# Kernel optimization log

Hardware: AMD Instinct MI355X
Metric: run time of the kernel (lower is better)

Reference implementation:

```python
import jax, jax.numpy as jnp
import numpy as np

B, LH, LP = 128, 64, 8
COV, TRE, OUT = 16, 8, 4
H = 128
H2 = 2 * H  # SDE latent dim
THETA, MU_SDE, SIGMA = 1.0, 0.0, 0.5
DT = 0.05
SUB = 20  # substeps per unit time interval (dt=0.05)
NSTEPS = (LP - 1) * SUB
EPS = 1e-5


def _tstats(x):
    # stats over the time axis (dim_to_normalize=-2)
    return x.mean(axis=1, keepdims=True), x.std(axis=1, keepdims=True)


def _ln(x):
    m = x.mean(-1, keepdims=True)
    v = ((x - m) ** 2).mean(-1, keepdims=True)
    return (x - m) * jax.lax.rsqrt(v + EPS)


def _gru_dir(x, Wih, Whh, bih, bhh):
    # x: (B, L, I); torch GRU gate order r, z, n
    gi_all = jnp.einsum('blc,gc->blg', x, Wih) + bih  # (B, L, 3H)

    def step(h, gi):
        gh = h @ Whh.T + bhh
        ir, iz, inn = jnp.split(gi, 3, axis=-1)
        hr, hz, hn = jnp.split(gh, 3, axis=-1)
        r = jax.nn.sigmoid(ir + hr)
        z = jax.nn.sigmoid(iz + hz)
        n = jnp.tanh(inn + r * hn)
        return (1.0 - z) * n + z * h, None

    h0 = jnp.zeros((x.shape[0], Whh.shape[1]), x.dtype)
    hT, _ = jax.lax.scan(step, h0, jnp.swapaxes(gi_all, 0, 1))
    return hT


def _bigru_hidden(x, Wf, Uf, bf, cf, Wb, Ub, bb, cb):
    # bidirectional GRU, hidden.mean(0) over the two directions
    return 0.5 * (_gru_dir(x, Wf, Uf, bf, cf) + _gru_dir(x[:, ::-1], Wb, Ub, bb, cb))


def _drift(y, mlp):
    # MLP [2H,4H,4H,2H], Linear -> Tanh -> LayerNorm per layer
    for W, b, g, be in mlp:
        y = _ln(jnp.tanh(y @ W.T + b)) * g + be
    return y


def setup_inputs():
    key = jax.random.key(0)
    ki = iter(jax.random.split(key, 64))
    nx = lambda shape, s=1.0: jax.random.normal(next(ki), shape, jnp.float32) * s
    d = {}
    d['covariate_history'] = nx((B, LH, COV))
    d['treatment_history'] = nx((B, LH, TRE))
    d['outcome_history'] = nx((B, LH, OUT))
    d['treatments'] = nx((B, LP, TRE))
    d['outcomes'] = nx((B, LP, OUT))
    for pre, insz in (('enc', COV + TRE + OUT), ('dec', TRE)):
        for suf in ('f', 'b'):
            d[f'{pre}_Wih_{suf}'] = nx((3 * H, insz), 0.05)
            d[f'{pre}_Whh_{suf}'] = nx((3 * H, H), 0.05)
            d[f'{pre}_bih_{suf}'] = jnp.zeros((3 * H,), jnp.float32)
            d[f'{pre}_bhh_{suf}'] = jnp.zeros((3 * H,), jnp.float32)
    dims = [H2, 2 * H2, 2 * H2, H2]
    for i in range(3):
        d[f'mlp_W{i}'] = nx((dims[i + 1], dims[i]), 0.05)
        d[f'mlp_b{i}'] = jnp.zeros((dims[i + 1],), jnp.float32)
        d[f'mlp_g{i}'] = jnp.ones((dims[i + 1],), jnp.float32)
        d[f'mlp_be{i}'] = jnp.zeros((dims[i + 1],), jnp.float32)
    d['out_W'] = nx((2 * OUT, H), 0.05)
    d['out_b'] = jnp.zeros((2 * OUT,), jnp.float32)
    d['ln_var_w'] = jnp.ones((OUT,), jnp.float32)
    d['ln_var_b'] = jnp.zeros((OUT,), jnp.float32)
    d['noise'] = nx((NSTEPS, B, H2))  # Brownian increments (pre-drawn)
    return d


def reference(covariate_history, treatment_history, outcome_history, treatments, outcomes,
              enc_Wih_f, enc_Whh_f, enc_bih_f, enc_bhh_f, enc_Wih_b, enc_Whh_b, enc_bih_b, enc_bhh_b,
              dec_Wih_f, dec_Whh_f, dec_bih_f, dec_bhh_f, dec_Wih_b, dec_Whh_b, dec_bih_b, dec_bhh_b,
              mlp_W0, mlp_b0, mlp_g0, mlp_be0, mlp_W1, mlp_b1, mlp_g1, mlp_be1,
              mlp_W2, mlp_b2, mlp_g2, mlp_be2, out_W, out_b, ln_var_w, ln_var_b, noise):
    # fixed (non-learned) time-axis normalizations
    om, os_ = _tstats(outcome_history)
    oh = (outcome_history - om) / (os_ + EPS)
    tm, ts_ = _tstats(treatment_history)
    tr = (treatments - tm) / (ts_ + EPS)
    th = (treatment_history - tm) / (ts_ + EPS)
    cm, cs = _tstats(covariate_history)
    ch = (covariate_history - cm) / (cs + EPS)

    enc_in = jnp.concatenate([ch, th, oh], axis=-1)  # (B, LH, COV+TRE+OUT)
    enc_h = _bigru_hidden(enc_in, enc_Wih_f, enc_Whh_f, enc_bih_f, enc_bhh_f,
                          enc_Wih_b, enc_Whh_b, enc_bih_b, enc_bhh_b)
    dec_h = _bigru_hidden(tr, dec_Wih_f, dec_Whh_f, dec_bih_f, dec_bhh_f,
                          dec_Wih_b, dec_Whh_b, dec_bih_b, dec_bhh_b)

    x0 = jnp.concatenate([enc_h, dec_h], axis=-1)  # (B, H2)
    aug0 = jnp.concatenate([x0, jnp.zeros((x0.shape[0], 1), x0.dtype)], axis=-1)
    mlp = ((mlp_W0, mlp_b0, mlp_g0, mlp_be0), (mlp_W1, mlp_b1, mlp_g1, mlp_be1),
           (mlp_W2, mlp_b2, mlp_g2, mlp_be2))
    sq = jnp.float32(np.sqrt(DT))

    def sde_step(y, nz):
        ys_ = y[:, :H2]
        f = _drift(ys_, mlp)
        u = (f - THETA * (MU_SDE - ys_)) / SIGMA
        flq = 0.5 * jnp.sum(u * u, axis=-1, keepdims=True)
        ynew = jnp.concatenate([ys_ + f * DT + (SIGMA * sq) * nz,
                                y[:, H2:] + flq * DT], axis=-1)
        return ynew, ynew

    _, traj = jax.lax.scan(sde_step, aug0, noise)
    ys = jnp.concatenate([aug0[None], traj[SUB - 1::SUB]], axis=0)  # (LP, B, H2+1)

    y = jnp.swapaxes(ys[..., :H], 0, 1)               # (B, LP, H) - first H dims only (as in source)
    logqp = jnp.transpose(ys[..., H:], (1, 2, 0))     # (B, H+1, LP)

    dec_out = y @ out_W.T + out_b                     # (B, LP, 2*OUT)
    mu_o, var_o = jnp.split(dec_out, 2, axis=-1)
    vm = var_o.mean(axis=1, keepdims=True)
    vv = var_o.var(axis=1, keepdims=True)
    var = jax.nn.sigmoid((var_o - vm) * jax.lax.rsqrt(vv + EPS) * ln_var_w + ln_var_b)
    mu = mu_o * (os_ + EPS) + om                      # inverse outcome normalization
    return (mu, var, logqp)
```

## Files before the change

kernel.cpp:

```cpp
#include <hip/hip_runtime.h>
#include <hip/hip_bf16.h>


#define EPS    1e-5f
#define DT_    0.05f
#define SQDT_  0.22360680997371674f
#define SIG_   0.5f

#define NB    128
#define NLH   64
#define NLP   8
#define NSTEP 140
#define NSUB  20

#define WSH_OFF   0
#define YS_OFF    65536
#define SLOT_OFF  504832

typedef __attribute__((ext_vector_type(8))) unsigned short ushort8;

__device__ __forceinline__ float bf2f(unsigned short u) {
  return __uint_as_float(((unsigned)u) << 16);
}
__device__ __forceinline__ float ldv(const void* p, int i, bool bf) {
  return bf ? bf2f(((const unsigned short*)p)[i]) : ((const float*)p)[i];
}
__device__ __forceinline__ void st_out(void* p, int i, float v, bool bf) {
  if (bf) ((__hip_bfloat16*)p)[i] = __float2bfloat16(v);
  else    ((float*)p)[i] = v;
}
__device__ __forceinline__ float sigm(float x) { return 1.f / (1.f + expf(-x)); }

template<int INSZ, int TSTEPS>
__device__ void gru_run(const float* xs, int rev,
                        const void* Wih, const void* Whh,
                        const void* bih, const void* bhh,
                        bool bf, float* hout,
                        float* h0, float* h1, float* rz)
{
  const int j = threadIdx.x;
  float whh[128];
  float wih[INSZ];
  if (bf) {
    const unsigned short* wp = (const unsigned short*)Whh;
    #pragma unroll
    for (int k = 0; k < 128; ++k) whh[k] = bf2f(wp[j*128 + k]);
    const unsigned short* ip = (const unsigned short*)Wih;
    #pragma unroll
    for (int c = 0; c < INSZ; ++c) wih[c] = bf2f(ip[j*INSZ + c]);
  } else {
    const float* wp = (const float*)Whh;
    #pragma unroll
    for (int k = 0; k < 128; ++k) whh[k] = wp[j*128 + k];
    const float* ip = (const float*)Wih;
    #pragma unroll
    for (int c = 0; c < INSZ; ++c) wih[c] = ip[j*INSZ + c];
  }
  const float bi = ldv(bih, j, bf);
  const float bh = ldv(bhh, j, bf);
  if (j < 128) h0[j] = 0.f;
  __syncthreads();

  #pragma unroll 1
  for (int it = 0; it < TSTEPS; ++it) {
    const float* hc = (it & 1) ? h1 : h0;
    float*       hn = (it & 1) ? h0 : h1;
    const int t = rev ? (TSTEPS - 1 - it) : it;
    float gh = bh;
    const float4* h4 = (const float4*)hc;
    #pragma unroll
    for (int k4 = 0; k4 < 32; ++k4) {
      const float4 hv = h4[k4];
      gh += whh[k4*4+0]*hv.x + whh[k4*4+1]*hv.y + whh[k4*4+2]*hv.z + whh[k4*4+3]*hv.w;
    }
    float gi = bi;
    #pragma unroll
    for (int c = 0; c < INSZ; ++c) gi += wih[c] * xs[t*INSZ + c];
    if (j < 256) rz[j] = sigm(gi + gh);
    __syncthreads();
    if (j >= 256) {
      const int i = j - 256;
      const float n = tanhf(gi + rz[i]*gh);
      const float z = rz[128 + i];
      hn[i] = (1.f - z)*n + z*hc[i];
    }
    __syncthreads();
  }
  const float* hf = (TSTEPS & 1) ? h1 : h0;
  if (j < 128) hout[j] = hf[j];
}

__global__ __launch_bounds__(384)
void k_gru_enc(const void* cov, const void* trh, const void* outh,
               const void* Wf, const void* Uf, const void* bf_, const void* cf_,
               const void* Wb, const void* Ub, const void* bb_, const void* cb_,
               float* ws, const void* lnvw)
{
  __shared__ __align__(16) float xs[NLH*28];
  __shared__ __align__(16) float h0[128], h1[128];
  __shared__ float rz[256];
  __shared__ float sm_[28], ss_[28];
  const bool bf = (((const unsigned*)lnvw)[0] != 0x3F800000u);
  const int bid = blockIdx.x;
  const int row = bid >> 1, back = bid & 1;
  const int tid = threadIdx.x;

  if (bid == 0) {
    unsigned* slots = (unsigned*)(ws + SLOT_OFF);
    for (int e = tid; e < 4096; e += 384) slots[e] = 0u;
  }
  if (tid < 28) {
    const void* src; int w; int f2;
    if (tid < 16)      { src = cov;  w = 16; f2 = tid; }
    else if (tid < 24) { src = trh;  w = 8;  f2 = tid - 16; }
    else               { src = outh; w = 4;  f2 = tid - 24; }
    float s1 = 0.f, s2 = 0.f;
    for (int t = 0; t < NLH; ++t) {
      const float v = ldv(src, (row*NLH + t)*w + f2, bf);
      s1 += v; s2 += v*v;
    }
    const float m = s1 / NLH;
    const float var = s2 / NLH - m*m;
    sm_[tid] = m;
    ss_[tid] = sqrtf(fmaxf(var, 0.f)) + EPS;
  }
  __syncthreads();
  for (int e = tid; e < NLH*28; e += 384) {
    const int t = e / 28, f2 = e % 28;
    const void* src; int w; int ff;
    if (f2 < 16)      { src = cov;  w = 16; ff = f2; }
    else if (f2 < 24) { src = trh;  w = 8;  ff = f2 - 16; }
    else              { src = outh; w = 4;  ff = f2 - 24; }
    const float v = ldv(src, (row*NLH + t)*w + ff, bf);
    xs[e] = (v - sm_[f2]) / ss_[f2];
  }
  __syncthreads();
  float* hout = ws + WSH_OFF + (row*4 + back)*128;
  if (back == 0) gru_run<28, NLH>(xs, 0, Wf, Uf, bf_, cf_, bf, hout, h0, h1, rz);
  else           gru_run<28, NLH>(xs, 1, Wb, Ub, bb_, cb_, bf, hout, h0, h1, rz);
}

__global__ __launch_bounds__(384)
void k_gru_dec(const void* trh, const void* trt,
               const void* Wf, const void* Uf, const void* bf_, const void* cf_,
               const void* Wb, const void* Ub, const void* bb_, const void* cb_,
               float* ws, const void* lnvw)
{
  __shared__ __align__(16) float xs[NLP*8];
  __shared__ __align__(16) float h0[128], h1[128];
  __shared__ float rz[256];
  __shared__ float sm_[8], ss_[8];
  const bool bf = (((const unsigned*)lnvw)[0] != 0x3F800000u);
  const int row = blockIdx.x >> 1, back = blockIdx.x & 1;
  const int tid = threadIdx.x;
  if (tid < 8) {
    float s1 = 0.f, s2 = 0.f;
    for (int t = 0; t < NLH; ++t) {
      const float v = ldv(trh, (row*NLH + t)*8 + tid, bf);
      s1 += v; s2 += v*v;
    }
    const float m = s1 / NLH;
    const float var = s2 / NLH - m*m;
    sm_[tid] = m;
    ss_[tid] = sqrtf(fmaxf(var, 0.f)) + EPS;
  }
  __syncthreads();
  for (int e = tid; e < NLP*8; e += 384) {
    const int t = e >> 3, f2 = e & 7;
    const float v = ldv(trt, (row*NLP + t)*8 + f2, bf);
    xs[e] = (v - sm_[f2]) / ss_[f2];
  }
  __syncthreads();
  float* hout = ws + WSH_OFF + (row*4 + 2 + back)*128;
  if (back == 0) gru_run<8, NLP>(xs, 0, Wf, Uf, bf_, cf_, bf, hout, h0, h1, rz);
  else           gru_run<8, NLP>(xs, 1, Wb, Ub, bb_, cb_, bf, hout, h0, h1, rz);
}

template<int N, int K>
__device__ __forceinline__ void mv_layer_bf(
    const unsigned short* W, const float* in, float* out,
    const float* bias, const float* gamma, const float* beta,
    float* red, int t, int lane, int wv, int g, int ks)
{
  constexpr int RPW = N/8;
  constexpr int NBT = RPW/8;
  constexpr int KI  = K/64;

  float4 xr[2*KI];
  #pragma unroll
  for (int kt = 0; kt < KI; ++kt) {
    xr[2*kt]   = *(const float4*)(in + kt*64 + ks*8);
    xr[2*kt+1] = *(const float4*)(in + kt*64 + ks*8 + 4);
  }
  const unsigned short* Wb0 = W + (wv*RPW + g)*K + ks*8;
  ushort8 wa[KI], wb[KI];
  #pragma unroll
  for (int kt = 0; kt < KI; ++kt) wa[kt] = *(const ushort8*)(Wb0 + kt*64);

  float ws1 = 0.f, ws2 = 0.f;
  #pragma unroll 1
  for (int b = 0; b < NBT; b += 2) {
    #pragma unroll
    for (int kt = 0; kt < KI; ++kt)
      wb[kt] = *(const ushort8*)(Wb0 + (b+1)*8*K + kt*64);
    {
      float a0 = 0.f, a1 = 0.f;
      #pragma unroll
      for (int kt = 0; kt < KI; ++kt) {
        const ushort8 w8 = wa[kt];
        const float4 xa = xr[2*kt], xb = xr[2*kt+1];
        a0 += bf2f(w8[0])*xa.x + bf2f(w8[1])*xa.y
            + bf2f(w8[2])*xa.z + bf2f(w8[3])*xa.w;
        a1 += bf2f(w8[4])*xb.x + bf2f(w8[5])*xb.y
            + bf2f(w8[6])*xb.z + bf2f(w8[7])*xb.w;
      }
      float acc = a0 + a1;
      acc += __shfl_xor(acc, 1, 64);
      acc += __shfl_xor(acc, 2, 64);
      acc += __shfl_xor(acc, 4, 64);
      const int row = wv*RPW + b*8 + g;
      const float v = tanhf(acc + bias[row]);
      if (ks == 0) { out[row] = v; ws1 += v; ws2 += v*v; }
    }
    if (b + 2 < NBT) {
      #pragma unroll
      for (int kt = 0; kt < KI; ++kt)
        wa[kt] = *(const ushort8*)(Wb0 + (b+2)*8*K + kt*64);
    }
    {
      float a0 = 0.f, a1 = 0.f;
      #pragma unroll
      for (int kt = 0; kt < KI; ++kt) {
        const ushort8 w8 = wb[kt];
        const float4 xa = xr[2*kt], xb = xr[2*kt+1];
        a0 += bf2f(w8[0])*xa.x + bf2f(w8[1])*xa.y
            + bf2f(w8[2])*xa.z + bf2f(w8[3])*xa.w;
        a1 += bf2f(w8[4])*xb.x + bf2f(w8[5])*xb.y
            + bf2f(w8[6])*xb.z + bf2f(w8[7])*xb.w;
      }
      float acc = a0 + a1;
      acc += __shfl_xor(acc, 1, 64);
      acc += __shfl_xor(acc, 2, 64);
      acc += __shfl_xor(acc, 4, 64);
      const int row = wv*RPW + (b+1)*8 + g;
      const float v = tanhf(acc + bias[row]);
      if (ks == 0) { out[row] = v; ws1 += v; ws2 += v*v; }
    }
  }
  #pragma unroll
  for (int off = 32; off >= 1; off >>= 1) {
    ws1 += __shfl_xor(ws1, off, 64);
    ws2 += __shfl_xor(ws2, off, 64);
  }
  if (lane == 0) { red[wv*2] = ws1; red[wv*2 + 1] = ws2; }
  __syncthreads();
  float t1 = 0.f, t2 = 0.f;
  #pragma unroll
  for (int q = 0; q < 8; ++q) { t1 += red[q*2]; t2 += red[q*2 + 1]; }
  const float m = t1/(float)N, var = t2/(float)N - m*m, rs = rsqrtf(var + EPS);
  if (t < N) out[t] = (out[t] - m)*rs*gamma[t] + beta[t];
  __syncthreads();
}

template<int N, int K>
__device__ __forceinline__ void mv_layer_f32(
    const float* W, const float* in, float* out,
    const float* bias, const float* gamma, const float* beta,
    float* red, int t, int lane, int wv, int g, int ks)
{
  constexpr int RPW = N/8;
  constexpr int NBT = RPW/8;
  constexpr int KI  = K/64;
  float ws1 = 0.f, ws2 = 0.f;
  #pragma unroll 1
  for (int b = 0; b < NBT; ++b) {
    const int row = wv*RPW + b*8 + g;
    const float* wr = W + row*K + ks*8;
    float a0 = 0.f, a1 = 0.f;
    #pragma unroll
    for (int kt = 0; kt < KI; ++kt) {
      const float4 w0 = *(const float4*)(wr + kt*64);
      const float4 w1 = *(const float4*)(wr + kt*64 + 4);
      const float4 xa = *(const float4*)(in + kt*64 + ks*8);
      const float4 xb = *(const float4*)(in + kt*64 + ks*8 + 4);
      a0 += w0.x*xa.x + w0.y*xa.y + w0.z*xa.z + w0.w*xa.w;
      a1 += w1.x*xb.x + w1.y*xb.y + w1.z*xb.z + w1.w*xb.w;
    }
    float acc = a0 + a1;
    acc += __shfl_xor(acc, 1, 64);
    acc += __shfl_xor(acc, 2, 64);
    acc += __shfl_xor(acc, 4, 64);
    const float v = tanhf(acc + bias[row]);
    if (ks == 0) { out[row] = v; ws1 += v; ws2 += v*v; }
  }
  #pragma unroll
  for (int off = 32; off >= 1; off >>= 1) {
    ws1 += __shfl_xor(ws1, off, 64);
    ws2 += __shfl_xor(ws2, off, 64);
  }
  if (lane == 0) { red[wv*2] = ws1; red[wv*2 + 1] = ws2; }
  __syncthreads();
  float t1 = 0.f, t2 = 0.f;
  #pragma unroll
  for (int q = 0; q < 8; ++q) { t1 += red[q*2]; t2 += red[q*2 + 1]; }
  const float m = t1/(float)N, var = t2/(float)N - m*m, rs = rsqrtf(var + EPS);
  if (t < N) out[t] = (out[t] - m)*rs*gamma[t] + beta[t];
  __syncthreads();
}

__global__ __launch_bounds__(512)
void k_sde(float* ws,
           const void* W0, const void* b0, const void* g0, const void* be0,
           const void* W1, const void* b1, const void* g1, const void* be1,
           const void* W2, const void* b2, const void* g2, const void* be2,
           const void* noise, const void* lnvw)
{
  __shared__ __align__(16) float xs[256];
  __shared__ __align__(16) float act1[512];
  __shared__ __align__(16) float act2[512];
  __shared__ __align__(16) float fC[256];
  __shared__ float prm[3840];
  __shared__ float red[16];
  __shared__ float lacc_s;

  const bool bf = (((const unsigned*)lnvw)[0] != 0x3F800000u);
  const int row = blockIdx.x;
  const int t = threadIdx.x;
  const int lane = t & 63, wv = t >> 6;
  const int g = lane >> 3, ks = lane & 7;

  float* bA = prm;        float* gA = prm +  512; float* beA = prm + 1024;
  float* bB = prm + 1536; float* gB = prm + 2048; float* beB = prm + 2560;
  float* bC = prm + 3072; float* gC = prm + 3328; float* beC = prm + 3584;
  bA[t] = ldv(b0, t, bf); gA[t] = ldv(g0, t, bf); beA[t] = ldv(be0, t, bf);
  bB[t] = ldv(b1, t, bf); gB[t] = ldv(g1, t, bf); beB[t] = ldv(be1, t, bf);
  if (t < 256) { bC[t] = ldv(b2, t, bf); gC[t] = ldv(g2, t, bf); beC[t] = ldv(be2, t, bf); }

  const float* wsh = ws + WSH_OFF;
  if (t < 256) {
    float v;
    if (t < 128) v = 0.5f*(wsh[(row*4 + 0)*128 + t]       + wsh[(row*4 + 1)*128 + t]);
    else         v = 0.5f*(wsh[(row*4 + 2)*128 + (t-128)] + wsh[(row*4 + 3)*128 + (t-128)]);
    xs[t] = v;
  }
  if (t == 0) lacc_s = 0.f;
  __syncthreads();
  float* ysw = ws + YS_OFF;
  if (t < 257) ysw[(row*8 + 0)*257 + t] = (t < 256) ? xs[t] : 0.f;

  #pragma unroll 1
  for (int s = 0; s < NSTEP; ++s) {
    float nzv = 0.f;
    if (t < 256) nzv = ldv(noise, ((s*NB) + row)*256 + t, bf);

    if (bf) {
      mv_layer_bf<512, 256>((const unsigned short*)W0, xs,   act1, bA, gA, beA, red, t, lane, wv, g, ks);
      mv_layer_bf<512, 512>((const unsigned short*)W1, act1, act2, bB, gB, beB, red, t, lane, wv, g, ks);
      mv_layer_bf<256, 512>((const unsigned short*)W2, act2, fC,   bC, gC, beC, red, t, lane, wv, g, ks);
    } else {
      mv_layer_f32<512, 256>((const float*)W0, xs,   act1, bA, gA, beA, red, t, lane, wv, g, ks);
      mv_layer_f32<512, 512>((const float*)W1, act1, act2, bB, gB, beB, red, t, lane, wv, g, ks);
      mv_layer_f32<256, 512>((const float*)W2, act2, fC,   bC, gC, beC, red, t, lane, wv, g, ks);
    }

    float u2 = 0.f;
    if (t < 256) {
      const float ysv = xs[t];
      const float fv  = fC[t];
      const float uu  = fv + ysv;
      u2 = uu*uu;
      xs[t] = ysv + fv*DT_ + SIG_*SQDT_*nzv;
    }
    float s1 = u2;
    #pragma unroll
    for (int off = 32; off >= 1; off >>= 1) s1 += __shfl_xor(s1, off, 64);
    if (lane == 0) red[wv*2] = s1;
    __syncthreads();
    if (t == 0) {
      float tot = 0.f;
      #pragma unroll
      for (int q = 0; q < 8; ++q) tot += red[q*2];
      lacc_s += 2.f*tot*DT_;
    }
    __syncthreads();
    if (((s + 1) % NSUB) == 0) {
      const int smp = (s + 1)/NSUB;
      if (t < 257) ysw[(row*8 + smp)*257 + t] = (t < 256) ? xs[t] : lacc_s;
    }
  }
}

__global__ __launch_bounds__(128)
void k_epi(const float* ws, const void* outh,
           const void* outW, const void* outB,
           const void* lvw, const void* lvb,
           void* d_out)
{
  __shared__ __align__(16) float ysl[8*257];
  __shared__ __align__(16) float ow[8*128];
  __shared__ float dout[64];
  __shared__ float om4[4], os4[4], vmv[4], vrs[4], ob[8], lw[4], lb[4];
  const bool bf = (((const unsigned*)lvw)[0] != 0x3F800000u);
  const int row = blockIdx.x, tid = threadIdx.x;
  const float* ysw = ws + YS_OFF + row*(8*257);
  for (int e = tid; e < 8*257; e += 128) ysl[e] = ysw[e];
  for (int e = tid; e < 1024; e += 128)  ow[e]  = ldv(outW, e, bf);
  if (tid < 8) ob[tid] = ldv(outB, tid, bf);
  if (tid < 4) { lw[tid] = ldv(lvw, tid, bf); lb[tid] = ldv(lvb, tid, bf); }
  if (tid < 4) {
    float s1 = 0.f, s2 = 0.f;
    for (int t = 0; t < NLH; ++t) {
      const float v = ldv(outh, (row*NLH + t)*4 + tid, bf);
      s1 += v; s2 += v*v;
    }
    const float m = s1 / NLH;
    const float var = s2 / NLH - m*m;
    om4[tid] = m;
    os4[tid] = sqrtf(fmaxf(var, 0.f)) + EPS;
  }
  __syncthreads();
  if (tid < 64) {
    const int smp = tid >> 3, o = tid & 7;
    float a = ob[o];
    #pragma unroll
    for (int k = 0; k < 128; ++k) a += ysl[smp*257 + k]*ow[o*128 + k];
    dout[smp*8 + o] = a;
  }
  __syncthreads();
  if (tid < 4) {
    float s1 = 0.f, s2 = 0.f;
    #pragma unroll
    for (int smp = 0; smp < 8; ++smp) { const float v = dout[smp*8 + 4 + tid]; s1 += v; s2 += v*v; }
    const float m = s1 / 8.f;
    const float var = s2 / 8.f - m*m;
    vmv[tid] = m;
    vrs[tid] = rsqrtf(var + EPS);
  }
  __syncthreads();
  if (tid < 32) {
    const int smp = tid >> 2, j = tid & 3;
    const float mu = dout[smp*8 + j]*os4[j] + om4[j];
    st_out(d_out, (row*8 + smp)*4 + j, mu, bf);
    const float vo = dout[smp*8 + 4 + j];
    const float vr = sigm((vo - vmv[j])*vrs[j]*lw[j] + lb[j]);
    st_out(d_out, 4096 + (row*8 + smp)*4 + j, vr, bf);
  }
  for (int e = tid; e < 129*8; e += 128) {
    const int j = e >> 3, smp = e & 7;
    st_out(d_out, 8192 + (row*129 + j)*8 + smp, ysl[smp*257 + 128 + j], bf);
  }
}

extern "C" void kernel_launch(void* const* d_in, const int* in_sizes, int n_in,
                              void* d_out, int out_size, void* d_ws, size_t ws_size,
                              hipStream_t stream) {
  (void)in_sizes; (void)n_in; (void)out_size; (void)ws_size;
  float* ws = (float*)d_ws;
  const void* lnvw = d_in[35];

  k_gru_enc<<<256, 384, 0, stream>>>(
      d_in[0], d_in[1], d_in[2],
      d_in[5], d_in[6], d_in[7], d_in[8],
      d_in[9], d_in[10], d_in[11], d_in[12],
      ws, lnvw);
  k_gru_dec<<<256, 384, 0, stream>>>(
      d_in[1], d_in[3],
      d_in[13], d_in[14], d_in[15], d_in[16],
      d_in[17], d_in[18], d_in[19], d_in[20],
      ws, lnvw);
  k_sde<<<128, 512, 0, stream>>>(
      ws,
      d_in[21], d_in[22], d_in[23], d_in[24],
      d_in[25], d_in[26], d_in[27], d_in[28],
      d_in[29], d_in[30], d_in[31], d_in[32],
      d_in[37], lnvw);
  k_epi<<<128, 128, 0, stream>>>(
      (const float*)d_ws, d_in[2],
      d_in[33], d_in[34], d_in[35], d_in[36],
      d_out);
}
```

Before: 2.968 ms.

## Use 16 waves per SDE block and defer tanh to one lane per row

The SDE kernel now launches 1024 threads per batch row instead of 512. Each wave handles 4 rows at a time with 16 lanes splitting K, where before it handled 8 rows with 8 lanes. Each finished dot product is parked in the lane whose kq index matches the row block, so tanh and the LayerNorm statistics run once per lane after the loop instead of inside every iteration. This aims to add latency hiding and cut serial work per wave in the 140-step recurrence, at the cost of an extra shuffle stage, more waves contending in the block barriers, and higher register pressure under the 1024-thread launch bound.

```diff
diff --git a/kernel.cpp b/kernel.cpp
--- a/kernel.cpp
+++ b/kernel.cpp
@@ -176,77 +176,108 @@
   else           gru_run<8, NLP>(xs, 1, Wb, Ub, bb_, cb_, bf, hout, h0, h1, rz);
 }
 
-template<int N, int K>
-__device__ __forceinline__ void mv_layer_bf(
-    const unsigned short* W, const float* in, float* out,
+template<int N, int K, bool BF>
+__device__ __forceinline__ void mv_layer(
+    const void* W, const float* in, float* out,
     const float* bias, const float* gamma, const float* beta,
-    float* red, int t, int lane, int wv, int g, int ks)
-{
-  constexpr int RPW = N/8;
-  constexpr int NBT = RPW/8;
-  constexpr int KI  = K/64;
+    float* red, int t, int lane, int wv, int rg, int kq)
+{
+  constexpr int WAVES = 16;
+  constexpr int RPW = N/WAVES;
+  constexpr int NBT = RPW/4;
+  constexpr int KI  = K/128;
 
   float4 xr[2*KI];
   #pragma unroll
   for (int kt = 0; kt < KI; ++kt) {
-    xr[2*kt]   = *(const float4*)(in + kt*64 + ks*8);
-    xr[2*kt+1] = *(const float4*)(in + kt*64 + ks*8 + 4);
-  }
-  const unsigned short* Wb0 = W + (wv*RPW + g)*K + ks*8;
-  ushort8 wa[KI], wb[KI];
-  #pragma unroll
-  for (int kt = 0; kt < KI; ++kt) wa[kt] = *(const ushort8*)(Wb0 + kt*64);
-
-  float ws1 = 0.f, ws2 = 0.f;
-  #pragma unroll 1
-  for (int b = 0; b < NBT; b += 2) {
-    #pragma unroll
-    for (int kt = 0; kt < KI; ++kt)
-      wb[kt] = *(const ushort8*)(Wb0 + (b+1)*8*K + kt*64);
-    {
+    xr[2*kt]   = *(const float4*)(in + kt*128 + kq*8);
+    xr[2*kt+1] = *(const float4*)(in + kt*128 + kq*8 + 4);
+  }
+
+  float pk = 0.f;
+  if (BF) {
+    const unsigned short* Wb0 = (const unsigned short*)W + (wv*RPW + rg)*K + kq*8;
+    ushort8 wa[KI], wb[KI];
+    #pragma unroll
+    for (int kt = 0; kt < KI; ++kt) wa[kt] = *(const ushort8*)(Wb0 + kt*128);
+    #pragma unroll 1
+    for (int b = 0; b < NBT; b += 2) {
+      #pragma unroll
+      for (int kt = 0; kt < KI; ++kt)
+        wb[kt] = *(const ushort8*)(Wb0 + (b+1)*4*K + kt*128);
+      {
+        float a0 = 0.f, a1 = 0.f;
+        #pragma unroll
+        for (int kt = 0; kt < KI; ++kt) {
+          const ushort8 w8 = wa[kt];
+          const float4 xa = xr[2*kt], xb = xr[2*kt+1];
+          a0 += bf2f(w8[0])*xa.x + bf2f(w8[1])*xa.y
+              + bf2f(w8[2])*xa.z + bf2f(w8[3])*xa.w;
+          a1 += bf2f(w8[4])*xb.x + bf2f(w8[5])*xb.y
+              + bf2f(w8[6])*xb.z + bf2f(w8[7])*xb.w;
+        }
+        float acc = a0 + a1;
+        acc += __shfl_xor(acc, 1, 64);
+        acc += __shfl_xor(acc, 2, 64);
+        acc += __shfl_xor(acc, 4, 64);
+        acc += __shfl_xor(acc, 8, 64);
+        const float val = acc + bias[wv*RPW + b*4 + rg];
+        pk = (kq == b) ? val : pk;
+      }
+      if (b + 2 < NBT) {
+        #pragma unroll
+        for (int kt = 0; kt < KI; ++kt)
+          wa[kt] = *(const ushort8*)(Wb0 + (b+2)*4*K + kt*128);
+      }
+      {
+        float a0 = 0.f, a1 = 0.f;
+        #pragma unroll
+        for (int kt = 0; kt < KI; ++kt) {
+          const ushort8 w8 = wb[kt];
+          const float4 xa = xr[2*kt], xb = xr[2*kt+1];
+          a0 += bf2f(w8[0])*xa.x + bf2f(w8[1])*xa.y
+              + bf2f(w8[2])*xa.z + bf2f(w8[3])*xa.w;
+          a1 += bf2f(w8[4])*xb.x + bf2f(w8[5])*xb.y
+              + bf2f(w8[6])*xb.z + bf2f(w8[7])*xb.w;
+        }
+        float acc = a0 + a1;
+        acc += __shfl_xor(acc, 1, 64);
+        acc += __shfl_xor(acc, 2, 64);
+        acc += __shfl_xor(acc, 4, 64);
+        acc += __shfl_xor(acc, 8, 64);
+        const float val = acc + bias[wv*RPW + (b+1)*4 + rg];
+        pk = (kq == b + 1) ? val : pk;
+      }
+    }
+  } else {
+    const float* Wf0 = (const float*)W + (wv*RPW + rg)*K + kq*8;
+    #pragma unroll 1
+    for (int b = 0; b < NBT; ++b) {
+      const float* wr = Wf0 + b*4*K;
       float a0 = 0.f, a1 = 0.f;
       #pragma unroll
       for (int kt = 0; kt < KI; ++kt) {
-        const ushort8 w8 = wa[kt];
+        const float4 w0 = *(const float4*)(wr + kt*128);
+        const float4 w1 = *(const float4*)(wr + kt*128 + 4);
         const float4 xa = xr[2*kt], xb = xr[2*kt+1];
-        a0 += bf2f(w8[0])*xa.x + bf2f(w8[1])*xa.y
-            + bf2f(w8[2])*xa.z + bf2f(w8[3])*xa.w;
-        a1 += bf2f(w8[4])*xb.x + bf2f(w8[5])*xb.y
-            + bf2f(w8[6])*xb.z + bf2f(w8[7])*xb.w;
+        a0 += w0.x*xa.x + w0.y*xa.y + w0.z*xa.z + w0.w*xa.w;
+        a1 += w1.x*xb.x + w1.y*xb.y + w1.z*xb.z + w1.w*xb.w;
       }
       float acc = a0 + a1;
       acc += __shfl_xor(acc, 1, 64);
       acc += __shfl_xor(acc, 2, 64);
       acc += __shfl_xor(acc, 4, 64);
-      const int row = wv*RPW + b*8 + g;
-      const float v = tanhf(acc + bias[row]);
-      if (ks == 0) { out[row] = v; ws1 += v; ws2 += v*v; }
-    }
-    if (b + 2 < NBT) {
-      #pragma unroll
-      for (int kt = 0; kt < KI; ++kt)
-        wa[kt] = *(const ushort8*)(Wb0 + (b+2)*8*K + kt*64);
-    }
-    {
-      float a0 = 0.f, a1 = 0.f;
-      #pragma unroll
-      for (int kt = 0; kt < KI; ++kt) {
-        const ushort8 w8 = wb[kt];
-        const float4 xa = xr[2*kt], xb = xr[2*kt+1];
-        a0 += bf2f(w8[0])*xa.x + bf2f(w8[1])*xa.y
-            + bf2f(w8[2])*xa.z + bf2f(w8[3])*xa.w;
-        a1 += bf2f(w8[4])*xb.x + bf2f(w8[5])*xb.y
-            + bf2f(w8[6])*xb.z + bf2f(w8[7])*xb.w;
-      }
-      float acc = a0 + a1;
-      acc += __shfl_xor(acc, 1, 64);
-      acc += __shfl_xor(acc, 2, 64);
-      acc += __shfl_xor(acc, 4, 64);
-      const int row = wv*RPW + (b+1)*8 + g;
-      const float v = tanhf(acc + bias[row]);
-      if (ks == 0) { out[row] = v; ws1 += v; ws2 += v*v; }
-    }
-  }
+      acc += __shfl_xor(acc, 8, 64);
+      const float val = acc + bias[wv*RPW + b*4 + rg];
+      pk = (kq == b) ? val : pk;
+    }
+  }
+
+  const float v = tanhf(pk);
+  const bool own = (kq < NBT);
+  float ws1 = own ? v : 0.f;
+  float ws2 = own ? v*v : 0.f;
+  if (own) out[wv*RPW + kq*4 + rg] = v;
   #pragma unroll
   for (int off = 32; off >= 1; off >>= 1) {
     ws1 += __shfl_xor(ws1, off, 64);
@@ -256,59 +287,13 @@
   __syncthreads();
   float t1 = 0.f, t2 = 0.f;
   #pragma unroll
-  for (int q = 0; q < 8; ++q) { t1 += red[q*2]; t2 += red[q*2 + 1]; }
+  for (int q = 0; q < WAVES; ++q) { t1 += red[q*2]; t2 += red[q*2 + 1]; }
   const float m = t1/(float)N, var = t2/(float)N - m*m, rs = rsqrtf(var + EPS);
   if (t < N) out[t] = (out[t] - m)*rs*gamma[t] + beta[t];
   __syncthreads();
 }
 
-template<int N, int K>
-__device__ __forceinline__ void mv_layer_f32(
-    const float* W, const float* in, float* out,
-    const float* bias, const float* gamma, const float* beta,
-    float* red, int t, int lane, int wv, int g, int ks)
-{
-  constexpr int RPW = N/8;
-  constexpr int NBT = RPW/8;
-  constexpr int KI  = K/64;
-  float ws1 = 0.f, ws2 = 0.f;
-  #pragma unroll 1
-  for (int b = 0; b < NBT; ++b) {
-    const int row = wv*RPW + b*8 + g;
-    const float* wr = W + row*K + ks*8;
-    float a0 = 0.f, a1 = 0.f;
-    #pragma unroll
-    for (int kt = 0; kt < KI; ++kt) {
-      const float4 w0 = *(const float4*)(wr + kt*64);
-      const float4 w1 = *(const float4*)(wr + kt*64 + 4);
-      const float4 xa = *(const float4*)(in + kt*64 + ks*8);
-      const float4 xb = *(const float4*)(in + kt*64 + ks*8 + 4);
-      a0 += w0.x*xa.x + w0.y*xa.y + w0.z*xa.z + w0.w*xa.w;
-      a1 += w1.x*xb.x + w1.y*xb.y + w1.z*xb.z + w1.w*xb.w;
-    }
-    float acc = a0 + a1;
-    acc += __shfl_xor(acc, 1, 64);
-    acc += __shfl_xor(acc, 2, 64);
-    acc += __shfl_xor(acc, 4, 64);
-    const float v = tanhf(acc + bias[row]);
-    if (ks == 0) { out[row] = v; ws1 += v; ws2 += v*v; }
-  }
-  #pragma unroll
-  for (int off = 32; off >= 1; off >>= 1) {
-    ws1 += __shfl_xor(ws1, off, 64);
-    ws2 += __shfl_xor(ws2, off, 64);
-  }
-  if (lane == 0) { red[wv*2] = ws1; red[wv*2 + 1] = ws2; }
-  __syncthreads();
-  float t1 = 0.f, t2 = 0.f;
-  #pragma unroll
-  for (int q = 0; q < 8; ++q) { t1 += red[q*2]; t2 += red[q*2 + 1]; }
-  const float m = t1/(float)N, var = t2/(float)N - m*m, rs = rsqrtf(var + EPS);
-  if (t < N) out[t] = (out[t] - m)*rs*gamma[t] + beta[t];
-  __syncthreads();
-}
-
-__global__ __launch_bounds__(512)
+__global__ __launch_bounds__(1024)
 void k_sde(float* ws,
            const void* W0, const void* b0, const void* g0, const void* be0,
            const void* W1, const void* b1, const void* g1, const void* be1,
@@ -320,20 +305,22 @@
   __shared__ __align__(16) float act2[512];
   __shared__ __align__(16) float fC[256];
   __shared__ float prm[3840];
-  __shared__ float red[16];
+  __shared__ float red[32];
   __shared__ float lacc_s;
 
   const bool bf = (((const unsigned*)lnvw)[0] != 0x3F800000u);
   const int row = blockIdx.x;
   const int t = threadIdx.x;
   const int lane = t & 63, wv = t >> 6;
-  const int g = lane >> 3, ks = lane & 7;
+  const int rg = lane >> 4, kq = lane & 15;
 
   float* bA = prm;        float* gA = prm +  512; float* beA = prm + 1024;
   float* bB = prm + 1536; float* gB = prm + 2048; float* beB = prm + 2560;
   float* bC = prm + 3072; float* gC = prm + 3328; float* beC = prm + 3584;
-  bA[t] = ldv(b0, t, bf); gA[t] = ldv(g0, t, bf); beA[t] = ldv(be0, t, bf);
-  bB[t] = ldv(b1, t, bf); gB[t] = ldv(g1, t, bf); beB[t] = ldv(be1, t, bf);
+  if (t < 512) {
+    bA[t] = ldv(b0, t, bf); gA[t] = ldv(g0, t, bf); beA[t] = ldv(be0, t, bf);
+    bB[t] = ldv(b1, t, bf); gB[t] = ldv(g1, t, bf); beB[t] = ldv(be1, t, bf);
+  }
   if (t < 256) { bC[t] = ldv(b2, t, bf); gC[t] = ldv(g2, t, bf); beC[t] = ldv(be2, t, bf); }
 
   const float* wsh = ws + WSH_OFF;
@@ -354,13 +341,13 @@
     if (t < 256) nzv = ldv(noise, ((s*NB) + row)*256 + t, bf);
 
     if (bf) {
-      mv_layer_bf<512, 256>((const unsigned short*)W0, xs,   act1, bA, gA, beA, red, t, lane, wv, g, ks);
-      mv_layer_bf<512, 512>((const unsigned short*)W1, act1, act2, bB, gB, beB, red, t, lane, wv, g, ks);
-      mv_layer_bf<256, 512>((const unsigned short*)W2, act2, fC,   bC, gC, beC, red, t, lane, wv, g, ks);
+      mv_layer<512, 256, true>(W0, xs,   act1, bA, gA, beA, red, t, lane, wv, rg, kq);
+      mv_layer<512, 512, true>(W1, act1, act2, bB, gB, beB, red, t, lane, wv, rg, kq);
+      mv_layer<256, 512, true>(W2, act2, fC,   bC, gC, beC, red, t, lane, wv, rg, kq);
     } else {
-      mv_layer_f32<512, 256>((const float*)W0, xs,   act1, bA, gA, beA, red, t, lane, wv, g, ks);
-      mv_layer_f32<512, 512>((const float*)W1, act1, act2, bB, gB, beB, red, t, lane, wv, g, ks);
-      mv_layer_f32<256, 512>((const float*)W2, act2, fC,   bC, gC, beC, red, t, lane, wv, g, ks);
+      mv_layer<512, 256, false>(W0, xs,   act1, bA, gA, beA, red, t, lane, wv, rg, kq);
+      mv_layer<512, 512, false>(W1, act1, act2, bB, gB, beB, red, t, lane, wv, rg, kq);
+      mv_layer<256, 512, false>(W2, act2, fC,   bC, gC, beC, red, t, lane, wv, rg, kq);
     }
 
     float u2 = 0.f;
@@ -379,7 +366,7 @@
     if (t == 0) {
       float tot = 0.f;
       #pragma unroll
-      for (int q = 0; q < 8; ++q) tot += red[q*2];
+      for (int q = 0; q < 16; ++q) tot += red[q*2];
       lacc_s += 2.f*tot*DT_;
     }
     __syncthreads();
@@ -468,7 +455,7 @@
       d_in[13], d_in[14], d_in[15], d_in[16],
       d_in[17], d_in[18], d_in[19], d_in[20],
       ws, lnvw);
-  k_sde<<<128, 512, 0, stream>>>(
+  k_sde<<<128, 1024, 0, stream>>>(
       ws,
       d_in[21], d_in[22], d_in[23], d_in[24],
       d_in[25], d_in[26], d_in[27], d_in[28],
```

Measured after the change: 3.196 ms. 7.7% more time.
